# Kernel tuning notes

Measured on AMD Instinct MI355X. Metric: run time of the kernel, lower is better.

Reference implementation:

```python
import jax, jax.numpy as jnp
import numpy as np

V, E, H = 50000, 128, 256  # vocab, embedding_size, hidden_size
S, B = 512, 64             # seq_len, batch (seq-first, torch LSTM default)


def setup_inputs() -> dict:
    key = jax.random.key(0)
    ks = jax.random.split(key, 10)
    u = 1.0 / np.sqrt(H)  # torch LSTM/Linear init bound

    def unif(k, sh):
        return jax.random.uniform(k, sh, jnp.float32, -u, u)

    emb = jax.random.normal(ks[0], (V, E), jnp.float32) * 0.02
    emb = emb.at[0].set(0.0)  # padding_idx=0

    inp = {
        "seq": jax.random.randint(ks[1], (S, B), 0, V),
        "emb": emb,
        # forward direction weights (gate order i,f,g,o like torch)
        "W_ih_f": unif(ks[2], (4 * H, E)),
        "W_hh_f": unif(ks[3], (4 * H, H)),
        "b_f": unif(ks[4], (4 * H,)),  # b_ih + b_hh fused (identical math)
        # reverse direction
        "W_ih_b": unif(ks[5], (4 * H, E)),
        "W_hh_b": unif(ks[6], (4 * H, H)),
        "b_b": unif(ks[7], (4 * H,)),
        # classification head over concatenated bi-directional features
        "W_out": unif(ks[8], (1, 2 * H)),
        "b_out": unif(ks[9], (1,)),
    }
    return inp


def _lstm_scan(xg, W_hh):
    """xg: [S,B,4H] precomputed input-gate projections; returns hidden seq [S,B,H]."""
    b = xg.shape[1]
    h0 = jnp.zeros((b, H), xg.dtype)
    c0 = jnp.zeros((b, H), xg.dtype)

    def step(carry, xg_t):
        h, c = carry
        gates = xg_t + h @ W_hh.T  # [B,4H]
        i, f, g, o = jnp.split(gates, 4, axis=-1)
        i = jax.nn.sigmoid(i)
        f = jax.nn.sigmoid(f)
        g = jnp.tanh(g)
        o = jax.nn.sigmoid(o)
        c = f * c + i * g
        h = o * jnp.tanh(c)
        return (h, c), h

    _, hs = jax.lax.scan(step, (h0, c0), xg)
    return hs


def reference(seq, emb, W_ih_f, W_hh_f, b_f, W_ih_b, W_hh_b, b_b, W_out, b_out):
    # embedding with padding_idx=0 (row 0 contributes zero)
    x = jnp.where((seq == 0)[..., None], 0.0, emb[seq])  # [S,B,E]

    xg_f = jnp.einsum("sbe,ge->sbg", x, W_ih_f) + b_f          # [S,B,4H]
    hs_f = _lstm_scan(xg_f, W_hh_f)                             # [S,B,H]

    xr = x[::-1]
    xg_b = jnp.einsum("sbe,ge->sbg", xr, W_ih_b) + b_b
    hs_b = _lstm_scan(xg_b, W_hh_b)[::-1]                       # [S,B,H]

    out = jnp.concatenate([hs_f, hs_b], axis=-1)                # [S,B,2H]
    last = out[-1]                                              # [B,2H]
    return jax.nn.sigmoid(last @ W_out.T + b_out)               # [B,1]
```

## Files before the change

kernel.cpp:

```cpp
#include <hip/hip_runtime.h>
#include <hip/hip_bf16.h>
#include <stdint.h>
#include <string.h>

#define S_LEN 512
#define NBATCH 64
#define EDIM 128
#define HDIM 256
#define GDIM 1024

#define WQ_SCALE 1024.0f
#define HQ_SCALE 127.0f
#define LOG2E 1.4426950408889634f
#define C_IFO (-1.1093545e-05f)
#define C_G (2.2187090e-05f)

typedef __attribute__((ext_vector_type(8))) short short8;
typedef __attribute__((ext_vector_type(4))) short short4v;
typedef __attribute__((ext_vector_type(4))) float float4v;
typedef __attribute__((ext_vector_type(4))) int int4v;

#define OFF_WHH8 0u
#define SZ_WHH8 (256u * 64u * 16u)
#define OFF_WIH (OFF_WHH8 + SZ_WHH8)
#define SZ_WIH (64u * 4u * 64u * 16u)
#define OFF_XG ((size_t)(OFF_WIH + SZ_WIH))
#define SZ_XG ((size_t)S_LEN * NBATCH * GDIM * 2)
#define OFF_HF (OFF_XG + SZ_XG)

__device__ __forceinline__ short f2bf(float f) {
    union { float f; unsigned u; } v;
    v.f = f;
    unsigned r = (v.u + 0x7fffu + ((v.u >> 16) & 1u)) >> 16;
    return (short)r;
}
__device__ __forceinline__ float bf2f(short s) {
    union { unsigned u; float f; } v;
    v.u = ((unsigned)(unsigned short)s) << 16;
    return v.f;
}
__device__ __forceinline__ float sigm(float x) {
    float e = __expf(-x);
    return __builtin_amdgcn_rcpf(1.0f + e);
}
__device__ __forceinline__ float tanh_(float x) {
    float e = __expf(2.0f * x);
    return 1.0f - 2.0f * __builtin_amdgcn_rcpf(e + 1.0f);
}

__global__ __launch_bounds__(256) void setup_kernel(const float* __restrict__ whh_src,
                                                    const float* __restrict__ wih_src,
                                                    char* __restrict__ whh_dst,
                                                    char* __restrict__ wih_dst) {
    int bx = blockIdx.x;
    int tid = threadIdx.x;
    if (bx < 64) {
        int id = bx * 256 + tid;
        int lane = id & 63;
        int f = id >> 6;
        int tile = f >> 2, kc = f & 3;
        int row = tile * 16 + (lane & 15);
        int k0 = kc * 64 + ((lane >> 4) * 16);
        const float* s = whh_src + (size_t)row * HDIM + k0;
        union { char b[16]; int4v v; } u;
#pragma unroll
        for (int b = 0; b < 16; ++b)
            u.b[b] = (char)(int)rintf(s[b] * WQ_SCALE);
        *(int4v*)(whh_dst + ((size_t)f * 64 + lane) * 16) = u.v;
    } else {
        int id = (bx - 64) * 256 + tid;
        int lane = id & 63;
        int f = id >> 6;
        int tile = f >> 2;
        int c = f & 3;
        int row = tile * 16 + (lane & 15);
        int k0 = c * 32 + ((lane >> 4) * 8);
        const float* s = wih_src + (size_t)row * EDIM + k0;
        short8 pack;
#pragma unroll
        for (int j = 0; j < 8; ++j) pack[j] = f2bf(s[j]);
        *(short8*)(wih_dst + ((size_t)f * 64 + lane) * 16) = pack;
    }
}

__global__ __launch_bounds__(256) void input_proj(const int* __restrict__ seq,
                                                  const float* __restrict__ emb,
                                                  const char* __restrict__ wih_frags,
                                                  const float* __restrict__ bias,
                                                  char* __restrict__ xg) {
    __shared__ __align__(16) short lx[4][16][136];
    int tid = threadIdx.x;
    int t0 = blockIdx.x * 4;
    int g = blockIdx.y;

    {
        int row = tid >> 2;
        int tt = row >> 4, m = row & 15;
        int k0 = (tid & 3) * 32;
        int v = seq[(t0 + tt) * NBATCH + g * 16 + m];
        const float* src = emb + (size_t)v * EDIM + k0;
        bool zero = (v == 0);
#pragma unroll
        for (int u = 0; u < 32; u += 4) {
            float4v f = *(const float4v*)(src + u);
            short4v p;
#pragma unroll
            for (int e = 0; e < 4; ++e) p[e] = zero ? (short)0 : f2bf(f[e]);
            *(short4v*)&lx[tt][m][k0 + u] = p;
        }
    }
    __syncthreads();

    int lane = tid & 63, w = tid >> 6;
    int ln = lane & 15, q = lane >> 4;

    short8 Bx[4][4];
#pragma unroll
    for (int tt = 0; tt < 4; ++tt)
#pragma unroll
        for (int c = 0; c < 4; ++c)
            Bx[tt][c] = *(const short8*)&lx[tt][ln][c * 32 + q * 8];

    for (int nt = 0; nt < 16; ++nt) {
        int tile = w * 16 + nt;
        float kg = ((tile >> 4) == 2) ? (2.0f * LOG2E) : (-LOG2E);
        short8 Aw[4];
#pragma unroll
        for (int c = 0; c < 4; ++c)
            Aw[c] = *(const short8*)(wih_frags + (((size_t)tile * 4 + c) * 64 + lane) * 16);
        float4v b4 = *(const float4v*)(bias + tile * 16 + q * 4);
#pragma unroll
        for (int tt = 0; tt < 4; ++tt) {
            float4v acc = b4;
#pragma unroll
            for (int c = 0; c < 4; ++c)
                acc = __builtin_amdgcn_mfma_f32_16x16x32_bf16(Aw[c], Bx[tt][c], acc, 0, 0, 0);
            short4v p;
#pragma unroll
            for (int r = 0; r < 4; ++r) p[r] = f2bf(acc[r] * kg);
            size_t off = ((size_t)(t0 + tt) * NBATCH + g * 16 + ln) * GDIM + tile * 16 + q * 4;
            *(short4v*)(xg + off * 2) = p;
        }
    }
}

#define HPAD 320
__global__ __launch_bounds__(1024, 4) void lstm_scan(const char* __restrict__ whh8,
                                                     const char* __restrict__ xg,
                                                     float* __restrict__ hf_out) {
    __shared__ __align__(16) char hls[2][4][HPAD];
    int tid = threadIdx.x;
    int lane = tid & 63, w = tid >> 6;
    int ln = lane & 15, q = lane >> 4;
    int bg = blockIdx.x;

    int4v Wfr[4][4];
#pragma unroll
    for (int g = 0; g < 4; ++g) {
        int tile = g * 16 + w;
#pragma unroll
        for (int kc = 0; kc < 4; ++kc)
            Wfr[g][kc] = *(const int4v*)(whh8 + (((size_t)(tile * 4 + kc)) * 64 + lane) * 16);
    }

    {
        int* hp = (int*)&hls[0][0][0];
        for (int i = tid; i < (2 * 4 * HPAD) / 4; i += 1024) hp[i] = 0;
    }

    const char* hrd = &hls[0][0][0];
    char* hwr = &hls[1][0][0];
    int hoff_rd = (ln & 3) * HPAD + q * 16;

    int b = ln & 3;
    int rr = ln >> 2;
    int j = w * 16 + q * 4 + rr;
    int hoff_wr = b * HPAD + j;

    bool r_lo = (rr & 1) != 0;
    bool r_hi = (rr & 2) != 0;

    float cst = 0.0f;

    const char* xgp = xg + (((size_t)(bg * 4 + b) * GDIM + j) * 2);
    const size_t tstep = (size_t)NBATCH * GDIM * 2;

    unsigned short xq[4];
#pragma unroll
    for (int g = 0; g < 4; ++g)
        xq[g] = *(const unsigned short*)(xgp + g * 512);

    __syncthreads();

    const int4v z4 = {0, 0, 0, 0};
    for (int t = 0; t < S_LEN; ++t) {
        int4v Bh[4];
#pragma unroll
        for (int kc = 0; kc < 4; ++kc)
            Bh[kc] = *(const int4v*)(hrd + hoff_rd + kc * 64);

        float xgf[4];
#pragma unroll
        for (int g = 0; g < 4; ++g) xgf[g] = bf2f((short)xq[g]);
        xgp += tstep;
        if (t != S_LEN - 1) {
#pragma unroll
            for (int g = 0; g < 4; ++g)
                xq[g] = *(const unsigned short*)(xgp + g * 512);
        }

        int4v a[4];
#pragma unroll
        for (int g = 0; g < 4; ++g)
            a[g] = __builtin_amdgcn_mfma_i32_16x16x64_i8(Wfr[g][0], Bh[0], z4, 0, 0, 0);
#pragma unroll
        for (int kc = 1; kc < 4; ++kc)
#pragma unroll
            for (int g = 0; g < 4; ++g)
                a[g] = __builtin_amdgcn_mfma_i32_16x16x64_i8(Wfr[g][kc], Bh[kc], a[g], 0, 0, 0);

        int gsel[4];
#pragma unroll
        for (int g = 0; g < 4; ++g) {
            int v01 = r_lo ? a[g][1] : a[g][0];
            int v23 = r_lo ? a[g][3] : a[g][2];
            gsel[g] = r_hi ? v23 : v01;
        }
        float s0 = fmaf((float)gsel[0], C_IFO, xgf[0]);
        float s1 = fmaf((float)gsel[1], C_IFO, xgf[1]);
        float s2 = fmaf((float)gsel[2], C_G, xgf[2]);
        float s3 = fmaf((float)gsel[3], C_IFO, xgf[3]);

        float iv = __builtin_amdgcn_rcpf(1.0f + exp2f(s0));
        float fv = __builtin_amdgcn_rcpf(1.0f + exp2f(s1));
        float gv = fmaf(-2.0f, __builtin_amdgcn_rcpf(1.0f + exp2f(s2)), 1.0f);
        float ov = __builtin_amdgcn_rcpf(1.0f + exp2f(s3));
        float cv = fmaf(fv, cst, iv * gv);
        cst = cv;
        float tc = fmaf(-2.0f, __builtin_amdgcn_rcpf(1.0f + exp2f(cv * (2.0f * LOG2E))), 1.0f);
        float hv = ov * tc;

        int hq = (int)rintf(hv * HQ_SCALE);
        hwr[hoff_wr] = (char)hq;

        if (t == S_LEN - 1)
            hf_out[((size_t)(bg * 4 + b)) * HDIM + j] = hv;

        const char* tr = hrd; hrd = hwr; hwr = (char*)tr;
        __syncthreads();
    }
}

__global__ __launch_bounds__(256) void tail_kernel(const int* __restrict__ seq,
                                                   const float* __restrict__ emb,
                                                   const float* __restrict__ wih_b,
                                                   const float* __restrict__ b_b,
                                                   const float* __restrict__ wout,
                                                   const float* __restrict__ b_out,
                                                   const float* __restrict__ hf,
                                                   float* __restrict__ out) {
    __shared__ float xs[EDIM];
    __shared__ float red[4];
    int b = blockIdx.x, tid = threadIdx.x;
    if (tid < EDIM) {
        int v = seq[(S_LEN - 1) * NBATCH + b];
        xs[tid] = (v == 0) ? 0.0f : emb[(size_t)v * EDIM + tid];
    }
    __syncthreads();

    int j = tid;
    float si = b_b[j], sg = b_b[2 * HDIM + j], so = b_b[3 * HDIM + j];
    const float* wi = wih_b + (size_t)j * EDIM;
    const float* wg = wih_b + (size_t)(2 * HDIM + j) * EDIM;
    const float* wo = wih_b + (size_t)(3 * HDIM + j) * EDIM;
#pragma unroll 8
    for (int k = 0; k < EDIM; k += 4) {
        float4v x4 = *(const float4v*)&xs[k];
        float4v a = *(const float4v*)(wi + k);
        float4v c = *(const float4v*)(wg + k);
        float4v d = *(const float4v*)(wo + k);
#pragma unroll
        for (int e = 0; e < 4; ++e) {
            si += a[e] * x4[e];
            sg += c[e] * x4[e];
            so += d[e] * x4[e];
        }
    }
    float cc = sigm(si) * tanh_(sg);
    float hb = sigm(so) * tanh_(cc);
    float partial = hf[(size_t)b * HDIM + j] * wout[j] + hb * wout[HDIM + j];

    float val = partial;
#pragma unroll
    for (int off = 32; off > 0; off >>= 1) val += __shfl_down(val, off, 64);
    int lane = tid & 63, wv = tid >> 6;
    if (lane == 0) red[wv] = val;
    __syncthreads();
    if (tid == 0) out[b] = sigm(red[0] + red[1] + red[2] + red[3] + b_out[0]);
}

extern "C" void kernel_launch(void* const* d_in, const int* in_sizes, int n_in,
                              void* d_out, int out_size, void* d_ws, size_t ws_size,
                              hipStream_t stream) {
    const int* seq = (const int*)d_in[0];
    const float* emb = (const float*)d_in[1];
    const float* Wih_f = (const float*)d_in[2];
    const float* Whh_f = (const float*)d_in[3];
    const float* b_f = (const float*)d_in[4];
    const float* Wih_b = (const float*)d_in[5];
    const float* b_b = (const float*)d_in[7];
    const float* Wout = (const float*)d_in[8];
    const float* b_out = (const float*)d_in[9];
    float* out = (float*)d_out;
    char* ws = (char*)d_ws;

    setup_kernel<<<dim3(128), 256, 0, stream>>>(Whh_f, Wih_f, ws + OFF_WHH8, ws + OFF_WIH);
    input_proj<<<dim3(S_LEN / 4, 4), 256, 0, stream>>>(seq, emb, ws + OFF_WIH, b_f, ws + OFF_XG);
    lstm_scan<<<dim3(16), 1024, 0, stream>>>(ws + OFF_WHH8, ws + OFF_XG, (float*)(ws + OFF_HF));
    tail_kernel<<<dim3(NBATCH), 256, 0, stream>>>(seq, emb, Wih_b, b_b, Wout, b_out,
                                                  (const float*)(ws + OFF_HF), out);
}
```

Measured before the change: 626.7 us.

## Replace per-step block barrier with split LDS atomic counters in LSTM scan

Removes the __syncthreads at the end of each recurrent step. Two workgroup-scope atomic counters, one per half of the hidden vector (waves 0-7 and 8-15), signal when each half of h has been written. Each wave spins on the first counter, loads the first two K-chunks of h and starts its MFMAs, then waits on the second counter for the remaining chunks. The goal is to overlap the second half's MFMAs with the slower waves and avoid a full-block stall each step, at the cost of spin-polling with s_sleep and extra atomic traffic, which can add latency of its own.

```diff
diff --git a/kernel.cpp b/kernel.cpp
--- a/kernel.cpp
+++ b/kernel.cpp
@@ -149,6 +149,7 @@
                                                      const char* __restrict__ xg,
                                                      float* __restrict__ hf_out) {
     __shared__ __align__(16) char hls[2][4][HPAD];
+    __shared__ int cnt[2];
     int tid = threadIdx.x;
     int lane = tid & 63, w = tid >> 6;
     int ln = lane & 15, q = lane >> 4;
@@ -166,6 +167,7 @@
     {
         int* hp = (int*)&hls[0][0][0];
         for (int i = tid; i < (2 * 4 * HPAD) / 4; i += 1024) hp[i] = 0;
+        if (tid < 2) cnt[tid] = 0;
     }
 
     const char* hrd = &hls[0][0][0];
@@ -180,6 +182,8 @@
     bool r_lo = (rr & 1) != 0;
     bool r_hi = (rr & 2) != 0;
 
+    int* my_cnt = &cnt[w >> 3];
+
     float cst = 0.0f;
 
     const char* xgp = xg + (((size_t)(bg * 4 + b) * GDIM + j) * 2);
@@ -194,10 +198,23 @@
 
     const int4v z4 = {0, 0, 0, 0};
     for (int t = 0; t < S_LEN; ++t) {
-        int4v Bh[4];
-#pragma unroll
-        for (int kc = 0; kc < 4; ++kc)
-            Bh[kc] = *(const int4v*)(hrd + hoff_rd + kc * 64);
+        int tgt = t * 8;
+
+        while (__hip_atomic_load(&cnt[0], __ATOMIC_ACQUIRE,
+                                 __HIP_MEMORY_SCOPE_WORKGROUP) < tgt)
+            __builtin_amdgcn_s_sleep(1);
+        __builtin_amdgcn_sched_barrier(0);
+
+        int4v Bh0 = *(const int4v*)(hrd + hoff_rd);
+        int4v Bh1 = *(const int4v*)(hrd + hoff_rd + 64);
+
+        int4v a[4];
+#pragma unroll
+        for (int g = 0; g < 4; ++g)
+            a[g] = __builtin_amdgcn_mfma_i32_16x16x64_i8(Wfr[g][0], Bh0, z4, 0, 0, 0);
+#pragma unroll
+        for (int g = 0; g < 4; ++g)
+            a[g] = __builtin_amdgcn_mfma_i32_16x16x64_i8(Wfr[g][1], Bh1, a[g], 0, 0, 0);
 
         float xgf[4];
 #pragma unroll
@@ -209,15 +226,19 @@
                 xq[g] = *(const unsigned short*)(xgp + g * 512);
         }
 
-        int4v a[4];
+        while (__hip_atomic_load(&cnt[1], __ATOMIC_ACQUIRE,
+                                 __HIP_MEMORY_SCOPE_WORKGROUP) < tgt)
+            __builtin_amdgcn_s_sleep(1);
+        __builtin_amdgcn_sched_barrier(0);
+
+        int4v Bh2 = *(const int4v*)(hrd + hoff_rd + 128);
+        int4v Bh3 = *(const int4v*)(hrd + hoff_rd + 192);
 #pragma unroll
         for (int g = 0; g < 4; ++g)
-            a[g] = __builtin_amdgcn_mfma_i32_16x16x64_i8(Wfr[g][0], Bh[0], z4, 0, 0, 0);
-#pragma unroll
-        for (int kc = 1; kc < 4; ++kc)
-#pragma unroll
-            for (int g = 0; g < 4; ++g)
-                a[g] = __builtin_amdgcn_mfma_i32_16x16x64_i8(Wfr[g][kc], Bh[kc], a[g], 0, 0, 0);
+            a[g] = __builtin_amdgcn_mfma_i32_16x16x64_i8(Wfr[g][2], Bh2, a[g], 0, 0, 0);
+#pragma unroll
+        for (int g = 0; g < 4; ++g)
+            a[g] = __builtin_amdgcn_mfma_i32_16x16x64_i8(Wfr[g][3], Bh3, a[g], 0, 0, 0);
 
         int gsel[4];
 #pragma unroll
@@ -246,8 +267,11 @@
         if (t == S_LEN - 1)
             hf_out[((size_t)(bg * 4 + b)) * HDIM + j] = hv;
 
+        if (lane == 0)
+            __hip_atomic_fetch_add(my_cnt, 1, __ATOMIC_RELEASE,
+                                   __HIP_MEMORY_SCOPE_WORKGROUP);
+
         const char* tr = hrd; hrd = hwr; hwr = (char*)tr;
-        __syncthreads();
     }
 }
 
```

Measured after the change: 652.8 us. 4.2% more time.
